# Kernel tuning notes

Measured on AMD Instinct MI355X. Metric: run time of the kernel, lower is better.

The kernel has to match this reference:

```python
import jax, jax.numpy as jnp
import numpy as np

B, T, D = 8, 128, 512


def setup_inputs() -> dict:
    key = jax.random.key(0)
    ks = jax.random.split(key, 13)
    s = 1.0 / np.sqrt(D)
    inp = {"x": jax.random.normal(ks[0], (B, T, D), dtype=jnp.float32)}
    names = ["qf", "kf", "vf", "qt", "kt", "vt"]
    for i, n in enumerate(names):
        inp[f"W_{n}"] = jax.random.uniform(ks[1 + 2 * i], (D, D), dtype=jnp.float32, minval=-s, maxval=s)
        inp[f"b_{n}"] = jax.random.uniform(ks[2 + 2 * i], (D,), dtype=jnp.float32, minval=-s, maxval=s)
    return inp


def reference(x, W_qf, b_qf, W_kf, b_kf, W_vf, b_vf, W_qt, b_qt, W_kt, b_kt, W_vt, b_vt):
    # torch nn.Linear stores weight as [out, in]: y = x @ W.T + b
    lin = lambda h, W, b: jnp.einsum('bti,oi->bto', h, W) + b

    # --- feature branch: elementwise Q*K scores, softmax over feature dim ---
    Q_f = lin(x, W_qf, b_qf)
    K_f = lin(x, W_kf, b_kf)
    V_f = lin(x, W_vf, b_vf)
    ctx_f = jax.nn.softmax(Q_f * K_f, axis=-1) * V_f  # [B,T,D]

    # --- temporal(-named) branch: per-(b,t) outer product over feature dim ---
    Q_t = lin(x, W_qt, b_qt)
    K_t = lin(x, W_kt, b_kt)
    V_t = lin(x, W_vt, b_vt)
    scores_t = jnp.einsum('bti,btj->btij', Q_t, K_t)          # [B,T,D,D]
    probs_t = jax.nn.softmax(scores_t, axis=-1)
    ctx_t = jnp.einsum('btij,btj->bti', probs_t, V_t)          # [B,T,D]

    # dropout is identity in eval mode
    return ctx_f + ctx_t
```

## Files before the change

### kernel.cpp

```cpp
#include <hip/hip_runtime.h>
#include <hip/hip_bf16.h>
#include <math.h>


#define M_ROWS 1024
#define DIMD   512
#define NCOLS  3072
#define KPHYS  1024

typedef __attribute__((ext_vector_type(8))) short short8;
typedef __attribute__((ext_vector_type(4))) float f32x4;
typedef __attribute__((ext_vector_type(4))) unsigned short u16x4;

struct PtrArgs {
    const float* W[6];
    const float* b[6];
};

#define XN (M_ROWS * DIMD)
#define WN (NCOLS * DIMD)

__device__ __forceinline__ unsigned short bf16_rne(float v) {
    unsigned u = __float_as_uint(v);
    u = (u + 0x7FFFu + ((u >> 16) & 1u)) >> 16;
    return (unsigned short)u;
}

__device__ __constant__ float INVFACT[25] = {
    1.0f, 1.0f, 0.5f,
    1.6666666666666666e-01f, 4.1666666666666664e-02f, 8.3333333333333332e-03f,
    1.3888888888888889e-03f, 1.9841269841269841e-04f, 2.4801587301587302e-05f,
    2.7557319223985893e-06f, 2.7557319223985888e-07f, 2.5052108385441720e-08f,
    2.0876756987868100e-09f, 1.6059043836821613e-10f, 1.1470745597729725e-11f,
    7.6471637318198164e-13f, 4.7794773323873853e-14f, 2.8114572543455206e-15f,
    1.5619206968586225e-16f, 8.2206352466243295e-18f, 4.1103176233121648e-19f,
    1.9572941063391263e-20f, 8.8967913924505741e-22f, 3.8681701706306835e-23f,
    1.6117375710961184e-24f
};

__global__ __launch_bounds__(256) void convert_split(const float* __restrict__ x,
                                                     PtrArgs pa,
                                                     unsigned short* __restrict__ Aph,
                                                     unsigned short* __restrict__ Bph,
                                                     float* __restrict__ biasAll) {
    const int idx = blockIdx.x * 256 + threadIdx.x;
    if (idx < NCOLS) {
        biasAll[idx] = pa.b[idx >> 9][idx & 511];
    }
    const int e4 = idx * 4;
    if (e4 < XN) {
        int m = e4 >> 9, k = e4 & 511;
        int s = k >> 5, p = k & 31;
        float4 v = *(const float4*)(x + e4);
        u16x4 hi, lo;
        hi.x = bf16_rne(v.x); lo.x = bf16_rne(v.x - __uint_as_float(((unsigned)hi.x) << 16));
        hi.y = bf16_rne(v.y); lo.y = bf16_rne(v.y - __uint_as_float(((unsigned)hi.y) << 16));
        hi.z = bf16_rne(v.z); lo.z = bf16_rne(v.z - __uint_as_float(((unsigned)hi.z) << 16));
        hi.w = bf16_rne(v.w); lo.w = bf16_rne(v.w - __uint_as_float(((unsigned)hi.w) << 16));
        *(u16x4*)&Aph[(size_t)m * KPHYS + s * 64 + p]      = hi;
        *(u16x4*)&Aph[(size_t)m * KPHYS + s * 64 + 32 + p] = lo;
    } else if (e4 < XN + WN) {
        int j = e4 - XN;
        int n = j >> 9, k = j & 511;
        int g = n >> 9, o = n & 511;
        int s = k >> 5, p = k & 31;
        float4 v = *(const float4*)(pa.W[g] + (size_t)o * DIMD + k);
        u16x4 hi, lo;
        hi.x = bf16_rne(v.x); lo.x = bf16_rne(v.x - __uint_as_float(((unsigned)hi.x) << 16));
        hi.y = bf16_rne(v.y); lo.y = bf16_rne(v.y - __uint_as_float(((unsigned)hi.y) << 16));
        hi.z = bf16_rne(v.z); lo.z = bf16_rne(v.z - __uint_as_float(((unsigned)hi.z) << 16));
        hi.w = bf16_rne(v.w); lo.w = bf16_rne(v.w - __uint_as_float(((unsigned)hi.w) << 16));
        *(u16x4*)&Bph[(size_t)n * KPHYS + s * 64 + p]      = hi;
        *(u16x4*)&Bph[(size_t)n * KPHYS + s * 64 + 32 + p] = lo;
    }
}

__global__ __launch_bounds__(256) void gemm_mfma(const unsigned short* __restrict__ A,
                                                 const unsigned short* __restrict__ B,
                                                 const float* __restrict__ biasAll,
                                                 float* __restrict__ Y) {
    __shared__ __align__(16) short As[2][64 * 64];
    __shared__ __align__(16) short Bs[2][128 * 64];

    const int tid  = threadIdx.x;
    const int m0   = blockIdx.y * 64;
    const int n0   = blockIdx.x * 128;
    const int lane = tid & 63;
    const int w    = tid >> 6;
    const int wm   = w & 1;
    const int wn   = w >> 1;
    const int l15  = lane & 15;
    const int quad = lane >> 4;

    f32x4 acc[2][4];
    #pragma unroll
    for (int i = 0; i < 2; ++i)
        #pragma unroll
        for (int j = 0; j < 4; ++j)
            acc[i][j] = (f32x4){0.f, 0.f, 0.f, 0.f};

    auto stage = [&](int it, int buf) {
        const int kbase = it * 64;
        #pragma unroll
        for (int t = 0; t < 2; ++t) {
            int idx = t * 256 + tid;
            int r = idx >> 3, c = idx & 7;
            int cc = c ^ (r & 7);
            const unsigned short* ga = A + (size_t)(m0 + r) * KPHYS + kbase + cc * 8;
            __builtin_amdgcn_global_load_lds(
                (const __attribute__((address_space(1))) unsigned int*)ga,
                (__attribute__((address_space(3))) unsigned int*)&As[buf][idx * 8], 16, 0, 0);
        }
        #pragma unroll
        for (int t = 0; t < 4; ++t) {
            int idx = t * 256 + tid;
            int r = idx >> 3, c = idx & 7;
            int cc = c ^ (r & 7);
            const unsigned short* gb = B + (size_t)(n0 + r) * KPHYS + kbase + cc * 8;
            __builtin_amdgcn_global_load_lds(
                (const __attribute__((address_space(1))) unsigned int*)gb,
                (__attribute__((address_space(3))) unsigned int*)&Bs[buf][idx * 8], 16, 0, 0);
        }
    };

    stage(0, 0);

    for (int it = 0; it < 16; ++it) {
        __syncthreads();
        if (it + 1 < 16) stage(it + 1, (it + 1) & 1);

        const short* as = As[it & 1];
        const short* bs = Bs[it & 1];
        short8 ah[2], al[2], bh[4], bl[4];
        #pragma unroll
        for (int mt = 0; mt < 2; ++mt) {
            int rA = wm * 32 + mt * 16 + l15;
            int ch = quad ^ (rA & 7);
            int cl = (4 + quad) ^ (rA & 7);
            ah[mt] = *(const short8*)&as[(rA * 8 + ch) * 8];
            al[mt] = *(const short8*)&as[(rA * 8 + cl) * 8];
        }
        #pragma unroll
        for (int nt = 0; nt < 4; ++nt) {
            int rB = wn * 64 + nt * 16 + l15;
            int ch = quad ^ (rB & 7);
            int cl = (4 + quad) ^ (rB & 7);
            bh[nt] = *(const short8*)&bs[(rB * 8 + ch) * 8];
            bl[nt] = *(const short8*)&bs[(rB * 8 + cl) * 8];
        }
        #pragma unroll
        for (int mt = 0; mt < 2; ++mt)
            #pragma unroll
            for (int nt = 0; nt < 4; ++nt) {
                acc[mt][nt] = __builtin_amdgcn_mfma_f32_16x16x32_bf16(
                    ah[mt], bh[nt], acc[mt][nt], 0, 0, 0);
                acc[mt][nt] = __builtin_amdgcn_mfma_f32_16x16x32_bf16(
                    ah[mt], bl[nt], acc[mt][nt], 0, 0, 0);
                acc[mt][nt] = __builtin_amdgcn_mfma_f32_16x16x32_bf16(
                    al[mt], bh[nt], acc[mt][nt], 0, 0, 0);
            }
    }

    #pragma unroll
    for (int nt = 0; nt < 4; ++nt) {
        int col = n0 + wn * 64 + nt * 16 + l15;
        float bv = biasAll[col];
        #pragma unroll
        for (int mt = 0; mt < 2; ++mt) {
            int row0 = m0 + wm * 32 + mt * 16 + quad * 4;
            #pragma unroll
            for (int r = 0; r < 4; ++r)
                Y[(size_t)(row0 + r) * NCOLS + col] = acc[mt][nt][r] + bv;
        }
    }
}

#define PSTR 53

__global__ __launch_bounds__(64) void fused_attn(const float* __restrict__ Y,
                                                 float* __restrict__ out) {
    const int row = blockIdx.x;
    const int l   = threadIdx.x;
    const float* __restrict__ Yr = Y + (size_t)row * NCOLS;
    const int i0 = l * 8;

    __shared__ float part[64 * PSTR];
    __shared__ float cbuf[50];

    const float LOG2E = 1.4426950408889634f;

    float4 qf0 = *(const float4*)(Yr + i0);
    float4 qf1 = *(const float4*)(Yr + i0 + 4);
    float4 kf0 = *(const float4*)(Yr + 512 + i0);
    float4 kf1 = *(const float4*)(Yr + 512 + i0 + 4);
    float4 vf0 = *(const float4*)(Yr + 1024 + i0);
    float4 vf1 = *(const float4*)(Yr + 1024 + i0 + 4);
    float4 qt0 = *(const float4*)(Yr + 1536 + i0);
    float4 qt1 = *(const float4*)(Yr + 1536 + i0 + 4);
    float4 kt0 = *(const float4*)(Yr + 2048 + i0);
    float4 kt1 = *(const float4*)(Yr + 2048 + i0 + 4);
    float4 vt0 = *(const float4*)(Yr + 2560 + i0);
    float4 vt1 = *(const float4*)(Yr + 2560 + i0 + 4);

    float e[8];
    e[0] = __builtin_amdgcn_exp2f(qf0.x * kf0.x * LOG2E);
    e[1] = __builtin_amdgcn_exp2f(qf0.y * kf0.y * LOG2E);
    e[2] = __builtin_amdgcn_exp2f(qf0.z * kf0.z * LOG2E);
    e[3] = __builtin_amdgcn_exp2f(qf0.w * kf0.w * LOG2E);
    e[4] = __builtin_amdgcn_exp2f(qf1.x * kf1.x * LOG2E);
    e[5] = __builtin_amdgcn_exp2f(qf1.y * kf1.y * LOG2E);
    e[6] = __builtin_amdgcn_exp2f(qf1.z * kf1.z * LOG2E);
    e[7] = __builtin_amdgcn_exp2f(qf1.w * kf1.w * LOG2E);
    float psum = ((e[0] + e[1]) + (e[2] + e[3])) + ((e[4] + e[5]) + (e[6] + e[7]));
    #pragma unroll
    for (int off = 32; off; off >>= 1) psum += __shfl_xor(psum, off);
    const float invS = 1.0f / psum;

    float k[8] = {kt0.x, kt0.y, kt0.z, kt0.w, kt1.x, kt1.y, kt1.z, kt1.w};
    float v[8] = {vt0.x, vt0.y, vt0.z, vt0.w, vt1.x, vt1.y, vt1.z, vt1.w};
    float kp[8] = {1.f, 1.f, 1.f, 1.f, 1.f, 1.f, 1.f, 1.f};
    float* myrow = &part[l * PSTR];
    #pragma unroll
    for (int p = 0; p < 25; ++p) {
        float n = ((kp[0] + kp[1]) + (kp[2] + kp[3])) +
                  ((kp[4] + kp[5]) + (kp[6] + kp[7]));
        float m = fmaf(kp[7], v[7], fmaf(kp[6], v[6],
                  fmaf(kp[5], v[5], fmaf(kp[4], v[4],
                  fmaf(kp[3], v[3], fmaf(kp[2], v[2],
                  fmaf(kp[1], v[1], kp[0] * v[0])))))));
        myrow[p]      = m;
        myrow[25 + p] = n;
        #pragma unroll
        for (int j = 0; j < 8; ++j) kp[j] *= k[j];
    }
    __syncthreads();

    if (l < 50) {
        float s = 0.f;
        #pragma unroll
        for (int i = 0; i < 64; ++i) s += part[i * PSTR + l];
        cbuf[l] = s * INVFACT[l < 25 ? l : l - 25];
    }
    __syncthreads();

    float q[8] = {qt0.x, qt0.y, qt0.z, qt0.w, qt1.x, qt1.y, qt1.z, qt1.w};
    float F[8], G[8];
    {
        float cf = cbuf[24], cg = cbuf[49];
        #pragma unroll
        for (int c = 0; c < 8; ++c) { F[c] = cf; G[c] = cg; }
    }
    #pragma unroll
    for (int p = 23; p >= 0; --p) {
        float cf = cbuf[p], cg = cbuf[25 + p];
        #pragma unroll
        for (int c = 0; c < 8; ++c) {
            F[c] = fmaf(F[c], q[c], cf);
            G[c] = fmaf(G[c], q[c], cg);
        }
    }

    float4 o0, o1;
    o0.x = e[0] * invS * vf0.x + F[0] / G[0];
    o0.y = e[1] * invS * vf0.y + F[1] / G[1];
    o0.z = e[2] * invS * vf0.z + F[2] / G[2];
    o0.w = e[3] * invS * vf0.w + F[3] / G[3];
    o1.x = e[4] * invS * vf1.x + F[4] / G[4];
    o1.y = e[5] * invS * vf1.y + F[5] / G[5];
    o1.z = e[6] * invS * vf1.z + F[6] / G[6];
    o1.w = e[7] * invS * vf1.w + F[7] / G[7];
    *(float4*)(out + (size_t)row * DIMD + i0)     = o0;
    *(float4*)(out + (size_t)row * DIMD + i0 + 4) = o1;
}

extern "C" void kernel_launch(void* const* d_in, const int* in_sizes, int n_in,
                              void* d_out, int out_size, void* d_ws, size_t ws_size,
                              hipStream_t stream) {
    const float* x = (const float*)d_in[0];
    PtrArgs pa;
    for (int g = 0; g < 6; ++g) {
        pa.W[g] = (const float*)d_in[1 + 2 * g];
        pa.b[g] = (const float*)d_in[2 + 2 * g];
    }

    char* ws = (char*)d_ws;
    float*          Y    = (float*)ws;
    unsigned short* Aph  = (unsigned short*)(ws + 12582912);
    unsigned short* Bph  = (unsigned short*)(ws + 12582912 + 2097152);
    float*          bias = (float*)(ws + 12582912 + 2097152 + 6291456);

    convert_split<<<(XN + WN) / 4 / 256, 256, 0, stream>>>(x, pa, Aph, Bph, bias);

    dim3 g1(NCOLS / 128, M_ROWS / 64);
    gemm_mfma<<<g1, 256, 0, stream>>>(Aph, Bph, bias, Y);

    fused_attn<<<M_ROWS, 64, 0, stream>>>(Y, (float*)d_out);
}
```

Before: 105.1 us.

## Merge convert, GEMM and attention into one cooperative kernel with grid syncs

Replaces three separate kernel launches with a single cooperative persistent kernel of 384 blocks that runs the bf16 split conversion, the MFMA GEMM and the fused attention epilogue, separated by grid-wide syncs. Shared memory is a union reused across phases, and the attention phase maps one row per wavefront with four rows per block. The aim is to remove inter-kernel launch gaps and tail effects. In exchange it adds grid-sync cost, caps the grid at 384 blocks, which reduces parallelism in the conversion and attention phases, and relies on in-wave LDS ordering without __syncthreads in the attention phase.

```diff
diff --git a/kernel.cpp b/kernel.cpp
--- a/kernel.cpp
+++ b/kernel.cpp
@@ -1,6 +1,9 @@
 #include <hip/hip_runtime.h>
+#include <hip/hip_cooperative_groups.h>
 #include <hip/hip_bf16.h>
 #include <math.h>
+
+namespace cg = cooperative_groups;
 
 
 #define M_ROWS 1024
@@ -19,6 +22,8 @@
 
 #define XN (M_ROWS * DIMD)
 #define WN (NCOLS * DIMD)
+#define NV4 ((XN + WN) / 4)
+#define NTHREADS (384 * 256)
 
 __device__ __forceinline__ unsigned short bf16_rne(float v) {
     unsigned u = __float_as_uint(v);
@@ -38,239 +43,253 @@
     1.6117375710961184e-24f
 };
 
-__global__ __launch_bounds__(256) void convert_split(const float* __restrict__ x,
-                                                     PtrArgs pa,
-                                                     unsigned short* __restrict__ Aph,
-                                                     unsigned short* __restrict__ Bph,
-                                                     float* __restrict__ biasAll) {
-    const int idx = blockIdx.x * 256 + threadIdx.x;
-    if (idx < NCOLS) {
-        biasAll[idx] = pa.b[idx >> 9][idx & 511];
+#define PSTR 53
+#define PWAVE (64 * PSTR + 56)
+
+union SMem {
+    struct {
+        short As[2][64 * 64];
+        short Bs[2][128 * 64];
+    } g;
+    struct {
+        float part[4][PWAVE];
+    } f;
+};
+
+__global__ __launch_bounds__(256, 2) void mega(const float* __restrict__ x,
+                                               PtrArgs pa,
+                                               unsigned short* __restrict__ Aph,
+                                               unsigned short* __restrict__ Bph,
+                                               float* __restrict__ biasAll,
+                                               float* __restrict__ Y,
+                                               float* __restrict__ out) {
+    cg::grid_group grid = cg::this_grid();
+    __shared__ __align__(16) SMem sm;
+
+    const int tid = threadIdx.x;
+    const int bid = blockIdx.x;
+
+    {
+        int gtid = bid * 256 + tid;
+        if (gtid < NCOLS) biasAll[gtid] = pa.b[gtid >> 9][gtid & 511];
+        for (int i = gtid; i < NV4; i += NTHREADS) {
+            const int e4 = i * 4;
+            if (e4 < XN) {
+                int m = e4 >> 9, k = e4 & 511;
+                int s = k >> 5, p = k & 31;
+                float4 v = *(const float4*)(x + e4);
+                u16x4 hi, lo;
+                hi.x = bf16_rne(v.x); lo.x = bf16_rne(v.x - __uint_as_float(((unsigned)hi.x) << 16));
+                hi.y = bf16_rne(v.y); lo.y = bf16_rne(v.y - __uint_as_float(((unsigned)hi.y) << 16));
+                hi.z = bf16_rne(v.z); lo.z = bf16_rne(v.z - __uint_as_float(((unsigned)hi.z) << 16));
+                hi.w = bf16_rne(v.w); lo.w = bf16_rne(v.w - __uint_as_float(((unsigned)hi.w) << 16));
+                *(u16x4*)&Aph[(size_t)m * KPHYS + s * 64 + p]      = hi;
+                *(u16x4*)&Aph[(size_t)m * KPHYS + s * 64 + 32 + p] = lo;
+            } else {
+                int j = e4 - XN;
+                int n = j >> 9, k = j & 511;
+                int g = n >> 9, o = n & 511;
+                int s = k >> 5, p = k & 31;
+                float4 v = *(const float4*)(pa.W[g] + (size_t)o * DIMD + k);
+                u16x4 hi, lo;
+                hi.x = bf16_rne(v.x); lo.x = bf16_rne(v.x - __uint_as_float(((unsigned)hi.x) << 16));
+                hi.y = bf16_rne(v.y); lo.y = bf16_rne(v.y - __uint_as_float(((unsigned)hi.y) << 16));
+                hi.z = bf16_rne(v.z); lo.z = bf16_rne(v.z - __uint_as_float(((unsigned)hi.z) << 16));
+                hi.w = bf16_rne(v.w); lo.w = bf16_rne(v.w - __uint_as_float(((unsigned)hi.w) << 16));
+                *(u16x4*)&Bph[(size_t)n * KPHYS + s * 64 + p]      = hi;
+                *(u16x4*)&Bph[(size_t)n * KPHYS + s * 64 + 32 + p] = lo;
+            }
+        }
     }
-    const int e4 = idx * 4;
-    if (e4 < XN) {
-        int m = e4 >> 9, k = e4 & 511;
-        int s = k >> 5, p = k & 31;
-        float4 v = *(const float4*)(x + e4);
-        u16x4 hi, lo;
-        hi.x = bf16_rne(v.x); lo.x = bf16_rne(v.x - __uint_as_float(((unsigned)hi.x) << 16));
-        hi.y = bf16_rne(v.y); lo.y = bf16_rne(v.y - __uint_as_float(((unsigned)hi.y) << 16));
-        hi.z = bf16_rne(v.z); lo.z = bf16_rne(v.z - __uint_as_float(((unsigned)hi.z) << 16));
-        hi.w = bf16_rne(v.w); lo.w = bf16_rne(v.w - __uint_as_float(((unsigned)hi.w) << 16));
-        *(u16x4*)&Aph[(size_t)m * KPHYS + s * 64 + p]      = hi;
-        *(u16x4*)&Aph[(size_t)m * KPHYS + s * 64 + 32 + p] = lo;
-    } else if (e4 < XN + WN) {
-        int j = e4 - XN;
-        int n = j >> 9, k = j & 511;
-        int g = n >> 9, o = n & 511;
-        int s = k >> 5, p = k & 31;
-        float4 v = *(const float4*)(pa.W[g] + (size_t)o * DIMD + k);
-        u16x4 hi, lo;
-        hi.x = bf16_rne(v.x); lo.x = bf16_rne(v.x - __uint_as_float(((unsigned)hi.x) << 16));
-        hi.y = bf16_rne(v.y); lo.y = bf16_rne(v.y - __uint_as_float(((unsigned)hi.y) << 16));
-        hi.z = bf16_rne(v.z); lo.z = bf16_rne(v.z - __uint_as_float(((unsigned)hi.z) << 16));
-        hi.w = bf16_rne(v.w); lo.w = bf16_rne(v.w - __uint_as_float(((unsigned)hi.w) << 16));
-        *(u16x4*)&Bph[(size_t)n * KPHYS + s * 64 + p]      = hi;
-        *(u16x4*)&Bph[(size_t)n * KPHYS + s * 64 + 32 + p] = lo;
-    }
-}
-
-__global__ __launch_bounds__(256) void gemm_mfma(const unsigned short* __restrict__ A,
-                                                 const unsigned short* __restrict__ B,
-                                                 const float* __restrict__ biasAll,
-                                                 float* __restrict__ Y) {
-    __shared__ __align__(16) short As[2][64 * 64];
-    __shared__ __align__(16) short Bs[2][128 * 64];
-
-    const int tid  = threadIdx.x;
-    const int m0   = blockIdx.y * 64;
-    const int n0   = blockIdx.x * 128;
-    const int lane = tid & 63;
-    const int w    = tid >> 6;
-    const int wm   = w & 1;
-    const int wn   = w >> 1;
-    const int l15  = lane & 15;
-    const int quad = lane >> 4;
-
-    f32x4 acc[2][4];
-    #pragma unroll
-    for (int i = 0; i < 2; ++i)
+    grid.sync();
+
+    {
+        const int m0   = (bid / 24) * 64;
+        const int n0   = (bid % 24) * 128;
+        const int lane = tid & 63;
+        const int w    = tid >> 6;
+        const int wm   = w & 1;
+        const int wn   = w >> 1;
+        const int l15  = lane & 15;
+        const int quad = lane >> 4;
+
+        f32x4 acc[2][4];
         #pragma unroll
-        for (int j = 0; j < 4; ++j)
-            acc[i][j] = (f32x4){0.f, 0.f, 0.f, 0.f};
-
-    auto stage = [&](int it, int buf) {
-        const int kbase = it * 64;
-        #pragma unroll
-        for (int t = 0; t < 2; ++t) {
-            int idx = t * 256 + tid;
-            int r = idx >> 3, c = idx & 7;
-            int cc = c ^ (r & 7);
-            const unsigned short* ga = A + (size_t)(m0 + r) * KPHYS + kbase + cc * 8;
-            __builtin_amdgcn_global_load_lds(
-                (const __attribute__((address_space(1))) unsigned int*)ga,
-                (__attribute__((address_space(3))) unsigned int*)&As[buf][idx * 8], 16, 0, 0);
+        for (int i = 0; i < 2; ++i)
+            #pragma unroll
+            for (int j = 0; j < 4; ++j)
+                acc[i][j] = (f32x4){0.f, 0.f, 0.f, 0.f};
+
+        auto stage = [&](int it, int buf) {
+            const int kbase = it * 64;
+            #pragma unroll
+            for (int t = 0; t < 2; ++t) {
+                int idx = t * 256 + tid;
+                int r = idx >> 3, c = idx & 7;
+                int cc = c ^ (r & 7);
+                const unsigned short* ga = Aph + (size_t)(m0 + r) * KPHYS + kbase + cc * 8;
+                __builtin_amdgcn_global_load_lds(
+                    (const __attribute__((address_space(1))) unsigned int*)ga,
+                    (__attribute__((address_space(3))) unsigned int*)&sm.g.As[buf][idx * 8], 16, 0, 0);
+            }
+            #pragma unroll
+            for (int t = 0; t < 4; ++t) {
+                int idx = t * 256 + tid;
+                int r = idx >> 3, c = idx & 7;
+                int cc = c ^ (r & 7);
+                const unsigned short* gb = Bph + (size_t)(n0 + r) * KPHYS + kbase + cc * 8;
+                __builtin_amdgcn_global_load_lds(
+                    (const __attribute__((address_space(1))) unsigned int*)gb,
+                    (__attribute__((address_space(3))) unsigned int*)&sm.g.Bs[buf][idx * 8], 16, 0, 0);
+            }
+        };
+
+        stage(0, 0);
+
+        for (int it = 0; it < 16; ++it) {
+            __syncthreads();
+            if (it + 1 < 16) stage(it + 1, (it + 1) & 1);
+
+            const short* as = sm.g.As[it & 1];
+            const short* bs = sm.g.Bs[it & 1];
+            short8 ah[2], al[2], bh[4], bl[4];
+            #pragma unroll
+            for (int mt = 0; mt < 2; ++mt) {
+                int rA = wm * 32 + mt * 16 + l15;
+                int ch = quad ^ (rA & 7);
+                int cl = (4 + quad) ^ (rA & 7);
+                ah[mt] = *(const short8*)&as[(rA * 8 + ch) * 8];
+                al[mt] = *(const short8*)&as[(rA * 8 + cl) * 8];
+            }
+            #pragma unroll
+            for (int nt = 0; nt < 4; ++nt) {
+                int rB = wn * 64 + nt * 16 + l15;
+                int ch = quad ^ (rB & 7);
+                int cl = (4 + quad) ^ (rB & 7);
+                bh[nt] = *(const short8*)&bs[(rB * 8 + ch) * 8];
+                bl[nt] = *(const short8*)&bs[(rB * 8 + cl) * 8];
+            }
+            #pragma unroll
+            for (int mt = 0; mt < 2; ++mt)
+                #pragma unroll
+                for (int nt = 0; nt < 4; ++nt) {
+                    acc[mt][nt] = __builtin_amdgcn_mfma_f32_16x16x32_bf16(
+                        ah[mt], bh[nt], acc[mt][nt], 0, 0, 0);
+                    acc[mt][nt] = __builtin_amdgcn_mfma_f32_16x16x32_bf16(
+                        ah[mt], bl[nt], acc[mt][nt], 0, 0, 0);
+                    acc[mt][nt] = __builtin_amdgcn_mfma_f32_16x16x32_bf16(
+                        al[mt], bh[nt], acc[mt][nt], 0, 0, 0);
+                }
         }
-        #pragma unroll
-        for (int t = 0; t < 4; ++t) {
-            int idx = t * 256 + tid;
-            int r = idx >> 3, c = idx & 7;
-            int cc = c ^ (r & 7);
-            const unsigned short* gb = B + (size_t)(n0 + r) * KPHYS + kbase + cc * 8;
-            __builtin_amdgcn_global_load_lds(
-                (const __attribute__((address_space(1))) unsigned int*)gb,
-                (__attribute__((address_space(3))) unsigned int*)&Bs[buf][idx * 8], 16, 0, 0);
-        }
-    };
-
-    stage(0, 0);
-
-    for (int it = 0; it < 16; ++it) {
-        __syncthreads();
-        if (it + 1 < 16) stage(it + 1, (it + 1) & 1);
-
-        const short* as = As[it & 1];
-        const short* bs = Bs[it & 1];
-        short8 ah[2], al[2], bh[4], bl[4];
-        #pragma unroll
-        for (int mt = 0; mt < 2; ++mt) {
-            int rA = wm * 32 + mt * 16 + l15;
-            int ch = quad ^ (rA & 7);
-            int cl = (4 + quad) ^ (rA & 7);
-            ah[mt] = *(const short8*)&as[(rA * 8 + ch) * 8];
-            al[mt] = *(const short8*)&as[(rA * 8 + cl) * 8];
-        }
+
         #pragma unroll
         for (int nt = 0; nt < 4; ++nt) {
-            int rB = wn * 64 + nt * 16 + l15;
-            int ch = quad ^ (rB & 7);
-            int cl = (4 + quad) ^ (rB & 7);
-            bh[nt] = *(const short8*)&bs[(rB * 8 + ch) * 8];
-            bl[nt] = *(const short8*)&bs[(rB * 8 + cl) * 8];
-        }
-        #pragma unroll
-        for (int mt = 0; mt < 2; ++mt)
-            #pragma unroll
-            for (int nt = 0; nt < 4; ++nt) {
-                acc[mt][nt] = __builtin_amdgcn_mfma_f32_16x16x32_bf16(
-                    ah[mt], bh[nt], acc[mt][nt], 0, 0, 0);
-                acc[mt][nt] = __builtin_amdgcn_mfma_f32_16x16x32_bf16(
-                    ah[mt], bl[nt], acc[mt][nt], 0, 0, 0);
-                acc[mt][nt] = __builtin_amdgcn_mfma_f32_16x16x32_bf16(
-                    al[mt], bh[nt], acc[mt][nt], 0, 0, 0);
-            }
-    }
-
-    #pragma unroll
-    for (int nt = 0; nt < 4; ++nt) {
-        int col = n0 + wn * 64 + nt * 16 + l15;
-        float bv = biasAll[col];
-        #pragma unroll
-        for (int mt = 0; mt < 2; ++mt) {
-            int row0 = m0 + wm * 32 + mt * 16 + quad * 4;
-            #pragma unroll
-            for (int r = 0; r < 4; ++r)
-                Y[(size_t)(row0 + r) * NCOLS + col] = acc[mt][nt][r] + bv;
+            int col = n0 + wn * 64 + nt * 16 + l15;
+            float bv = biasAll[col];
+            #pragma unroll
+            for (int mt = 0; mt < 2; ++mt) {
+                int row0 = m0 + wm * 32 + mt * 16 + quad * 4;
+                #pragma unroll
+                for (int r = 0; r < 4; ++r)
+                    Y[(size_t)(row0 + r) * NCOLS + col] = acc[mt][nt][r] + bv;
+            }
         }
     }
-}
-
-#define PSTR 53
-
-__global__ __launch_bounds__(64) void fused_attn(const float* __restrict__ Y,
-                                                 float* __restrict__ out) {
-    const int row = blockIdx.x;
-    const int l   = threadIdx.x;
-    const float* __restrict__ Yr = Y + (size_t)row * NCOLS;
-    const int i0 = l * 8;
-
-    __shared__ float part[64 * PSTR];
-    __shared__ float cbuf[50];
-
-    const float LOG2E = 1.4426950408889634f;
-
-    float4 qf0 = *(const float4*)(Yr + i0);
-    float4 qf1 = *(const float4*)(Yr + i0 + 4);
-    float4 kf0 = *(const float4*)(Yr + 512 + i0);
-    float4 kf1 = *(const float4*)(Yr + 512 + i0 + 4);
-    float4 vf0 = *(const float4*)(Yr + 1024 + i0);
-    float4 vf1 = *(const float4*)(Yr + 1024 + i0 + 4);
-    float4 qt0 = *(const float4*)(Yr + 1536 + i0);
-    float4 qt1 = *(const float4*)(Yr + 1536 + i0 + 4);
-    float4 kt0 = *(const float4*)(Yr + 2048 + i0);
-    float4 kt1 = *(const float4*)(Yr + 2048 + i0 + 4);
-    float4 vt0 = *(const float4*)(Yr + 2560 + i0);
-    float4 vt1 = *(const float4*)(Yr + 2560 + i0 + 4);
-
-    float e[8];
-    e[0] = __builtin_amdgcn_exp2f(qf0.x * kf0.x * LOG2E);
-    e[1] = __builtin_amdgcn_exp2f(qf0.y * kf0.y * LOG2E);
-    e[2] = __builtin_amdgcn_exp2f(qf0.z * kf0.z * LOG2E);
-    e[3] = __builtin_amdgcn_exp2f(qf0.w * kf0.w * LOG2E);
-    e[4] = __builtin_amdgcn_exp2f(qf1.x * kf1.x * LOG2E);
-    e[5] = __builtin_amdgcn_exp2f(qf1.y * kf1.y * LOG2E);
-    e[6] = __builtin_amdgcn_exp2f(qf1.z * kf1.z * LOG2E);
-    e[7] = __builtin_amdgcn_exp2f(qf1.w * kf1.w * LOG2E);
-    float psum = ((e[0] + e[1]) + (e[2] + e[3])) + ((e[4] + e[5]) + (e[6] + e[7]));
-    #pragma unroll
-    for (int off = 32; off; off >>= 1) psum += __shfl_xor(psum, off);
-    const float invS = 1.0f / psum;
-
-    float k[8] = {kt0.x, kt0.y, kt0.z, kt0.w, kt1.x, kt1.y, kt1.z, kt1.w};
-    float v[8] = {vt0.x, vt0.y, vt0.z, vt0.w, vt1.x, vt1.y, vt1.z, vt1.w};
-    float kp[8] = {1.f, 1.f, 1.f, 1.f, 1.f, 1.f, 1.f, 1.f};
-    float* myrow = &part[l * PSTR];
-    #pragma unroll
-    for (int p = 0; p < 25; ++p) {
-        float n = ((kp[0] + kp[1]) + (kp[2] + kp[3])) +
-                  ((kp[4] + kp[5]) + (kp[6] + kp[7]));
-        float m = fmaf(kp[7], v[7], fmaf(kp[6], v[6],
-                  fmaf(kp[5], v[5], fmaf(kp[4], v[4],
-                  fmaf(kp[3], v[3], fmaf(kp[2], v[2],
-                  fmaf(kp[1], v[1], kp[0] * v[0])))))));
-        myrow[p]      = m;
-        myrow[25 + p] = n;
-        #pragma unroll
-        for (int j = 0; j < 8; ++j) kp[j] *= k[j];
-    }
-    __syncthreads();
-
-    if (l < 50) {
-        float s = 0.f;
-        #pragma unroll
-        for (int i = 0; i < 64; ++i) s += part[i * PSTR + l];
-        cbuf[l] = s * INVFACT[l < 25 ? l : l - 25];
-    }
-    __syncthreads();
-
-    float q[8] = {qt0.x, qt0.y, qt0.z, qt0.w, qt1.x, qt1.y, qt1.z, qt1.w};
-    float F[8], G[8];
+    grid.sync();
+
     {
-        float cf = cbuf[24], cg = cbuf[49];
-        #pragma unroll
-        for (int c = 0; c < 8; ++c) { F[c] = cf; G[c] = cg; }
-    }
-    #pragma unroll
-    for (int p = 23; p >= 0; --p) {
-        float cf = cbuf[p], cg = cbuf[25 + p];
-        #pragma unroll
-        for (int c = 0; c < 8; ++c) {
-            F[c] = fmaf(F[c], q[c], cf);
-            G[c] = fmaf(G[c], q[c], cg);
+        const int w    = tid >> 6;
+        const int lane = tid & 63;
+        const int row  = w * 384 + bid;
+        if (row < M_ROWS) {
+            float* part = sm.f.part[w];
+            float* cbuf = part + 64 * PSTR;
+            const float* __restrict__ Yr = Y + (size_t)row * NCOLS;
+            const int i0 = lane * 8;
+            const float LOG2E = 1.4426950408889634f;
+
+            float4 qf0 = *(const float4*)(Yr + i0);
+            float4 qf1 = *(const float4*)(Yr + i0 + 4);
+            float4 kf0 = *(const float4*)(Yr + 512 + i0);
+            float4 kf1 = *(const float4*)(Yr + 512 + i0 + 4);
+            float4 vf0 = *(const float4*)(Yr + 1024 + i0);
+            float4 vf1 = *(const float4*)(Yr + 1024 + i0 + 4);
+            float4 qt0 = *(const float4*)(Yr + 1536 + i0);
+            float4 qt1 = *(const float4*)(Yr + 1536 + i0 + 4);
+            float4 kt0 = *(const float4*)(Yr + 2048 + i0);
+            float4 kt1 = *(const float4*)(Yr + 2048 + i0 + 4);
+            float4 vt0 = *(const float4*)(Yr + 2560 + i0);
+            float4 vt1 = *(const float4*)(Yr + 2560 + i0 + 4);
+
+            float e[8];
+            e[0] = __builtin_amdgcn_exp2f(qf0.x * kf0.x * LOG2E);
+            e[1] = __builtin_amdgcn_exp2f(qf0.y * kf0.y * LOG2E);
+            e[2] = __builtin_amdgcn_exp2f(qf0.z * kf0.z * LOG2E);
+            e[3] = __builtin_amdgcn_exp2f(qf0.w * kf0.w * LOG2E);
+            e[4] = __builtin_amdgcn_exp2f(qf1.x * kf1.x * LOG2E);
+            e[5] = __builtin_amdgcn_exp2f(qf1.y * kf1.y * LOG2E);
+            e[6] = __builtin_amdgcn_exp2f(qf1.z * kf1.z * LOG2E);
+            e[7] = __builtin_amdgcn_exp2f(qf1.w * kf1.w * LOG2E);
+            float psum = ((e[0] + e[1]) + (e[2] + e[3])) + ((e[4] + e[5]) + (e[6] + e[7]));
+            #pragma unroll
+            for (int off = 32; off; off >>= 1) psum += __shfl_xor(psum, off);
+            const float invS = 1.0f / psum;
+
+            float k[8] = {kt0.x, kt0.y, kt0.z, kt0.w, kt1.x, kt1.y, kt1.z, kt1.w};
+            float v[8] = {vt0.x, vt0.y, vt0.z, vt0.w, vt1.x, vt1.y, vt1.z, vt1.w};
+            float kp[8] = {1.f, 1.f, 1.f, 1.f, 1.f, 1.f, 1.f, 1.f};
+            float* myrow = &part[lane * PSTR];
+            #pragma unroll
+            for (int p = 0; p < 25; ++p) {
+                float n = ((kp[0] + kp[1]) + (kp[2] + kp[3])) +
+                          ((kp[4] + kp[5]) + (kp[6] + kp[7]));
+                float m = fmaf(kp[7], v[7], fmaf(kp[6], v[6],
+                          fmaf(kp[5], v[5], fmaf(kp[4], v[4],
+                          fmaf(kp[3], v[3], fmaf(kp[2], v[2],
+                          fmaf(kp[1], v[1], kp[0] * v[0])))))));
+                myrow[p]      = m;
+                myrow[25 + p] = n;
+                #pragma unroll
+                for (int j = 0; j < 8; ++j) kp[j] *= k[j];
+            }
+
+            if (lane < 50) {
+                float s = 0.f;
+                #pragma unroll
+                for (int i = 0; i < 64; ++i) s += part[i * PSTR + lane];
+                cbuf[lane] = s * INVFACT[lane < 25 ? lane : lane - 25];
+            }
+
+            float q[8] = {qt0.x, qt0.y, qt0.z, qt0.w, qt1.x, qt1.y, qt1.z, qt1.w};
+            float F[8], G[8];
+            {
+                float cf = cbuf[24], cg = cbuf[49];
+                #pragma unroll
+                for (int c = 0; c < 8; ++c) { F[c] = cf; G[c] = cg; }
+            }
+            #pragma unroll
+            for (int p = 23; p >= 0; --p) {
+                float cf = cbuf[p], cg = cbuf[25 + p];
+                #pragma unroll
+                for (int c = 0; c < 8; ++c) {
+                    F[c] = fmaf(F[c], q[c], cf);
+                    G[c] = fmaf(G[c], q[c], cg);
+                }
+            }
+
+            float4 o0, o1;
+            o0.x = e[0] * invS * vf0.x + F[0] / G[0];
+            o0.y = e[1] * invS * vf0.y + F[1] / G[1];
+            o0.z = e[2] * invS * vf0.z + F[2] / G[2];
+            o0.w = e[3] * invS * vf0.w + F[3] / G[3];
+            o1.x = e[4] * invS * vf1.x + F[4] / G[4];
+            o1.y = e[5] * invS * vf1.y + F[5] / G[5];
+            o1.z = e[6] * invS * vf1.z + F[6] / G[6];
+            o1.w = e[7] * invS * vf1.w + F[7] / G[7];
+            *(float4*)(out + (size_t)row * DIMD + i0)     = o0;
+            *(float4*)(out + (size_t)row * DIMD + i0 + 4) = o1;
         }
     }
-
-    float4 o0, o1;
-    o0.x = e[0] * invS * vf0.x + F[0] / G[0];
-    o0.y = e[1] * invS * vf0.y + F[1] / G[1];
-    o0.z = e[2] * invS * vf0.z + F[2] / G[2];
-    o0.w = e[3] * invS * vf0.w + F[3] / G[3];
-    o1.x = e[4] * invS * vf1.x + F[4] / G[4];
-    o1.y = e[5] * invS * vf1.y + F[5] / G[5];
-    o1.z = e[6] * invS * vf1.z + F[6] / G[6];
-    o1.w = e[7] * invS * vf1.w + F[7] / G[7];
-    *(float4*)(out + (size_t)row * DIMD + i0)     = o0;
-    *(float4*)(out + (size_t)row * DIMD + i0 + 4) = o1;
 }
 
 extern "C" void kernel_launch(void* const* d_in, const int* in_sizes, int n_in,
@@ -288,11 +307,10 @@
     unsigned short* Aph  = (unsigned short*)(ws + 12582912);
     unsigned short* Bph  = (unsigned short*)(ws + 12582912 + 2097152);
     float*          bias = (float*)(ws + 12582912 + 2097152 + 6291456);
-
-    convert_split<<<(XN + WN) / 4 / 256, 256, 0, stream>>>(x, pa, Aph, Bph, bias);
-
-    dim3 g1(NCOLS / 128, M_ROWS / 64);
-    gemm_mfma<<<g1, 256, 0, stream>>>(Aph, Bph, bias, Y);
-
-    fused_attn<<<M_ROWS, 64, 0, stream>>>(Y, (float*)d_out);
+    float*          out  = (float*)d_out;
+
+    void* args[] = {(void*)&x, (void*)&pa, (void*)&Aph, (void*)&Bph,
+                    (void*)&bias, (void*)&Y, (void*)&out};
+    hipLaunchCooperativeKernel((const void*)mega, dim3(384), dim3(256),
+                               args, 0, stream);
 }
```

After: 228.6 us. 118% more time.
